# Kernel tuning notes

Hardware: AMD Instinct MI355X
Metric: run time of the kernel (lower is better)

## Reference

```python
import jax, jax.numpy as jnp
import numpy as np

N_QUBITS = 14
N_LAYERS = 6
BATCH = 512
DIM = 2 ** N_QUBITS

# Z expectation sign table: qubit 0 is the most-significant bit of the state index
_idx = np.arange(DIM)
_bits = np.stack([(_idx >> (N_QUBITS - 1 - q)) & 1 for q in range(N_QUBITS)])  # [n, DIM]
SIGNS = jnp.asarray(1.0 - 2.0 * _bits, dtype=jnp.float32)  # +1 for bit 0, -1 for bit 1


def _rx(theta):
    # 2x2 RX(theta) = [[cos(t/2), -i sin(t/2)], [-i sin(t/2), cos(t/2)]]
    c = jnp.cos(theta / 2).astype(jnp.complex64)
    s = ((-1j) * jnp.sin(theta / 2)).astype(jnp.complex64)
    return jnp.stack([jnp.stack([c, s]), jnp.stack([s, c])])


def _apply_1q(state, mat, q):
    # state: [B, 2^n] complex; apply 2x2 mat on qubit q
    left = 2 ** q
    right = 2 ** (N_QUBITS - 1 - q)
    s = state.reshape(-1, left, 2, right)
    s = jnp.einsum('ij,bljr->blir', mat, s)
    return s.reshape(-1, DIM)


def _apply_cnot(state, c, t):
    # CNOT(control=c, target=t): flip target bit where control bit is 1
    hi, lo = (c, t) if c < t else (t, c)
    A = 2 ** hi
    M = 2 ** (lo - hi - 1)
    R = 2 ** (N_QUBITS - 1 - lo)
    s = state.reshape(-1, A, 2, M, 2, R)
    if c < t:
        flipped = jnp.flip(s[:, :, 1:2, :, :, :], axis=4)
        s = jnp.concatenate([s[:, :, 0:1, :, :, :], flipped], axis=2)
    else:
        flipped = jnp.flip(s[:, :, :, :, 1:2, :], axis=2)
        s = jnp.concatenate([s[:, :, :, :, 0:1, :], flipped], axis=4)
    return s.reshape(-1, DIM)


def _forward(x, params):
    B = x.shape[0]
    # angle embedding in X basis: product state of RX(x_q)|0> per qubit
    half = 0.5 * x
    amps = jnp.stack([jnp.cos(half).astype(jnp.complex64),
                      ((-1j) * jnp.sin(half)).astype(jnp.complex64)], axis=-1)  # [B, n, 2]
    state = amps[:, 0]
    for q in range(1, N_QUBITS):
        state = (state[:, :, None] * amps[:, q][:, None, :]).reshape(B, -1)
    # basic_entangling ansatz: per-qubit RX then ring of CNOTs, per layer
    for layer in range(N_LAYERS):
        w = params[layer, 0]  # [n_qubits]
        for q in range(N_QUBITS):
            state = _apply_1q(state, _rx(w[q]), q)
        for q in range(N_QUBITS):
            state = _apply_cnot(state, q, (q + 1) % N_QUBITS)
    # <Z_q> expectation per qubit
    probs = state.real ** 2 + state.imag ** 2  # [B, DIM]
    return probs @ SIGNS.T  # [B, n_qubits]


def setup_inputs():
    key = jax.random.key(0)
    k1, k2 = jax.random.split(key)
    x = jax.random.normal(k1, (BATCH, N_QUBITS), dtype=jnp.float32)
    params = 2.0 * jnp.pi * jax.random.uniform(k2, (N_LAYERS, 1, N_QUBITS), dtype=jnp.float32)
    return {"x": x, "params": params}


def reference(x, params):
    return _forward(x, params)
```

## Files before the change

### kernel.cpp

```cpp
#include <hip/hip_runtime.h>
#include <math.h>


#define NQ 14
#define DIM 16384
#define NLAYERS 6
#define NGATES (NLAYERS * NQ)
#define BATCH 512
#define TB 1024
#define NREP 16
#define NSLICE 16
#define SLICE_B (BATCH / NSLICE)
#define B_PER_WAVE (SLICE_B * 64 / TB)

constexpr int cpopc(unsigned v) { int c = 0; while (v) { c += (int)(v & 1u); v >>= 1; } return c; }

constexpr unsigned cpext(unsigned v, unsigned m) {
    unsigned r = 0; int b = 0;
    for (int pos = 0; pos < 16; ++pos)
        if ((m >> pos) & 1u) { r |= ((v >> pos) & 1u) << b; ++b; }
    return r;
}

struct Tabs {
    unsigned short m[NGATES];
    unsigned short r[NQ];
    int p[NQ];
    int off[NQ + 1];
    unsigned char qb[NQ][NQ];
    int ng[NQ];
    unsigned short gmask[NQ][NGATES];
    unsigned char  gidx[NQ][NGATES];
};

constexpr Tabs gen_tabs() {
    Tabs T{};
    unsigned short C[NQ] = {}, R[NQ] = {};
    for (int q = 0; q < NQ; ++q) { C[q] = (unsigned short)(1u << (NQ - 1 - q)); R[q] = C[q]; }
    for (int l = 0; l < NLAYERS; ++l) {
        for (int q = 0; q < NQ; ++q) T.m[l * NQ + q] = C[q];
        for (int g = 0; g < NQ; ++g) {
            int t = (g + 1) % NQ;
            C[g] ^= C[t];
            R[t] ^= R[g];
        }
    }
    for (int q = 0; q < NQ; ++q) T.r[q] = R[q];
    for (int q = 0; q < NQ; ++q) {
        int cnt = 0;
        for (int pos = 0; pos < NQ; ++pos)
            if ((R[q] >> pos) & 1u) { T.qb[q][cnt] = (unsigned char)(NQ - 1 - pos); ++cnt; }
        T.p[q] = cnt;
    }
    T.off[0] = 0;
    for (int q = 0; q < NQ; ++q) T.off[q + 1] = T.off[q] + (1 << T.p[q]);
    for (int q = 0; q < NQ; ++q) {
        int n = 0;
        for (int g = 0; g < NGATES; ++g) {
            if (cpopc((unsigned)(T.m[g] & R[q])) & 1) {
                T.gmask[q][n] = T.m[g];
                T.gidx[q][n]  = (unsigned char)g;
                ++n;
            }
        }
        T.ng[q] = n;
    }
    return T;
}
constexpr Tabs TAB = gen_tabs();

constexpr int calc_maxp() { int m = 0; for (int q = 0; q < NQ; ++q) if (TAB.p[q] > m) m = TAB.p[q]; return m; }
constexpr int calc_minp() { int m = 99; for (int q = 0; q < NQ; ++q) if (TAB.p[q] < m) m = TAB.p[q]; return m; }
constexpr int MAXP  = calc_maxp();
constexpr int MINP  = calc_minp();
constexpr int TOTAL = TAB.off[NQ];
static_assert(MAXP <= 8, "u = t & (2^p-1) needs p <= 10; replicas sized for p <= 8");
static_assert(MINP >= 1, "r mask must be nonzero");

template<int Q, int I>
__device__ __forceinline__ void gates(const float2* __restrict__ w, int t,
                                      float (&Bx)[16], float (&By)[16])
{
    if constexpr (I < TAB.ng[Q]) {
        constexpr unsigned r  = TAB.r[Q];
        constexpr unsigned nr = (~r) & 0x3FFFu;
        constexpr int      p  = TAB.p[Q];
        constexpr unsigned mg = TAB.gmask[Q][I];
        constexpr unsigned Ag = cpext(mg, r);
        constexpr unsigned Bg = cpext(mg, nr);
        constexpr unsigned Mg = Ag | ((Bg & ((1u << (10 - p)) - 1u)) << p);
        constexpr unsigned Hg = (Bg >> (10 - p)) & 15u;
        const float2 wv = w[I];
        const float si = (__popc((unsigned)t & Mg) & 1) ? -wv.y : wv.y;
        const float c  = wv.x;
        const float nx = Bx[Hg] * c - By[Hg] * si;
        const float ny = Bx[Hg] * si + By[Hg] * c;
        Bx[Hg] = nx; By[Hg] = ny;
        gates<Q, I + 1>(w, t, Bx, By);
    }
}

template<int Q>
__device__ __forceinline__ void build_q(const float2* __restrict__ w,
                                        float* __restrict__ binC,
                                        float* __restrict__ binS, int t)
{
    constexpr int      p       = TAB.p[Q];
    constexpr unsigned lowmask = (1u << p) - 1u;

    float Bx[16], By[16];
    #pragma unroll
    for (int h = 0; h < 16; ++h) { Bx[h] = 1.0f; By[h] = 0.0f; }
    gates<Q, 0>(w, t, Bx, By);

    #pragma unroll
    for (int s = 1; s < 4; s <<= 1) {
        #pragma unroll
        for (int h = 0; h < 16; ++h) {
            if (!(h & s)) {
                const int h1 = h | s;
                const float p1 = Bx[h] * Bx[h1], p2 = By[h] * By[h1];
                const float p3 = Bx[h] * By[h1], p4 = By[h] * Bx[h1];
                Bx[h]  = p1 - p2;  By[h]  = p3 + p4;
                Bx[h1] = p1 + p2;  By[h1] = p4 - p3;
            }
        }
    }
    #pragma unroll
    for (int h = 0; h < 4; ++h) {
        const int h1 = h | 4;
        const float p1 = Bx[h] * Bx[h1], p2 = By[h] * By[h1];
        const float p3 = Bx[h] * By[h1], p4 = By[h] * Bx[h1];
        Bx[h]  = p1 - p2;  By[h]  = p3 + p4;
        Bx[h1] = p1 + p2;  By[h1] = p4 - p3;
    }
    #pragma unroll
    for (int h = 8; h < 12; ++h) {
        const int h1 = h | 4;
        const float p1 = Bx[h] * Bx[h1], p2 = By[h] * By[h1];
        Bx[h]  = p1 - p2;
        Bx[h1] = p1 + p2;
    }

    float fx = 0.0f, fy = 0.0f;
    #pragma unroll
    for (int h = 0; h < 8; ++h) {
        fx = fmaf(Bx[h | 8], Bx[h], fx);
        fy = fmaf(Bx[h | 8], By[h], fy);
    }
    fx *= 2.0f; fy *= 2.0f;

    const unsigned u   = (unsigned)t & lowmask;
    const int      rep = t >> 6;
    float* bc = binC + (rep << MAXP);
    float* bs = binS + (rep << MAXP);

    if constexpr (p >= 6) {
        bc[u] = fx;
        bs[u] = fy;
    } else {
        constexpr unsigned dm = 63u & ~lowmask;
        #pragma unroll
        for (int bb = p; bb < 6; ++bb) {
            fx += __shfl_xor(fx, 1 << bb, 64);
            fy += __shfl_xor(fy, 1 << bb, 64);
        }
        if (((unsigned)t & dm) == 0u) {
            bc[u] = fx;
            bs[u] = fy;
        }
    }
}

template<int Q>
__device__ __forceinline__ void run_q(const float2* __restrict__ w,
                                      float* __restrict__ binC,
                                      float* __restrict__ binS,
                                      float2* __restrict__ tab2,
                                      const float* __restrict__ sxAll,
                                      float* __restrict__ out,
                                      int slice, int t)
{
    build_q<Q>(w, binC, binS, t);
    __syncthreads();

    constexpr int p  = TAB.p[Q];
    constexpr int nb = 1 << p;
    for (int i = t; i < nb; i += TB) {
        float sc = 0.0f, ss = 0.0f;
        #pragma unroll
        for (int rp = 0; rp < NREP; ++rp) {
            sc += binC[(rp << MAXP) + i];
            ss += binS[(rp << MAXP) + i];
        }
        tab2[i] = make_float2(sc, ss);
    }
    __syncthreads();

    const int wave = t >> 6;
    const int lane = t & 63;
    #pragma unroll
    for (int bb = 0; bb < B_PER_WAVE; ++bb) {
        const int bl = wave * B_PER_WAVE + bb;
        const float* xr = sxAll + bl * NQ;
        float xv[p];
        #pragma unroll
        for (int i = 0; i < p; ++i) xv[i] = xr[TAB.qb[Q][i]];

        float acc = 0.0f;
        if constexpr (p >= 6) {
            float A_low = 0.0f;
            #pragma unroll
            for (int i = 0; i < 6; ++i) A_low += ((lane >> i) & 1) ? xv[i] : -xv[i];
            constexpr int HI = 1 << (p - 6);
            #pragma unroll
            for (int j = 0; j < HI; ++j) {
                float A = A_low;
                #pragma unroll
                for (int i = 6; i < p; ++i) A += ((j >> (i - 6)) & 1) ? xv[i] : -xv[i];
                const int u = lane + (j << 6);
                float s, c;
                __sincosf(A, &s, &c);
                const float2 tv = tab2[u];
                acc = fmaf(c, tv.x, fmaf(s, tv.y, acc));
            }
        } else {
            if (lane < nb) {
                float A = 0.0f;
                #pragma unroll
                for (int i = 0; i < p; ++i) A += ((lane >> i) & 1) ? xv[i] : -xv[i];
                float s, c;
                __sincosf(A, &s, &c);
                const float2 tv = tab2[lane];
                acc = fmaf(c, tv.x, fmaf(s, tv.y, acc));
            }
        }

        #pragma unroll
        for (int o = 32; o > 0; o >>= 1)
            acc += __shfl_down(acc, o, 64);
        if (lane == 0)
            out[(slice * SLICE_B + bl) * NQ + Q] = acc * (1.0f / (float)DIM);
    }
}

__global__ __launch_bounds__(TB, 4)
void fused_kernel(const float* __restrict__ x, const float* __restrict__ params,
                  float* __restrict__ out)
{
    __shared__ float2 w[NGATES];
    __shared__ float  binC[NREP << MAXP];
    __shared__ float  binS[NREP << MAXP];
    __shared__ float2 tab2[1 << MAXP];
    __shared__ float  sxAll[SLICE_B * NQ];

    const int q     = blockIdx.x % NQ;
    const int slice = blockIdx.x / NQ;
    const int t     = threadIdx.x;
    const int ng    = TAB.ng[q];

    if (t < ng) {
        const float th = params[(int)TAB.gidx[q][t]];
        float s, c; sincosf(th, &s, &c);
        w[t] = make_float2(c, s);
    }
    for (int i = t; i < (NREP << MAXP); i += TB) { binC[i] = 0.0f; binS[i] = 0.0f; }
    for (int i = t; i < SLICE_B * NQ; i += TB)   sxAll[i] = x[slice * (SLICE_B * NQ) + i];
    __syncthreads();

    switch (q) {
        case 0:  run_q<0 >(w, binC, binS, tab2, sxAll, out, slice, t); break;
        case 1:  run_q<1 >(w, binC, binS, tab2, sxAll, out, slice, t); break;
        case 2:  run_q<2 >(w, binC, binS, tab2, sxAll, out, slice, t); break;
        case 3:  run_q<3 >(w, binC, binS, tab2, sxAll, out, slice, t); break;
        case 4:  run_q<4 >(w, binC, binS, tab2, sxAll, out, slice, t); break;
        case 5:  run_q<5 >(w, binC, binS, tab2, sxAll, out, slice, t); break;
        case 6:  run_q<6 >(w, binC, binS, tab2, sxAll, out, slice, t); break;
        case 7:  run_q<7 >(w, binC, binS, tab2, sxAll, out, slice, t); break;
        case 8:  run_q<8 >(w, binC, binS, tab2, sxAll, out, slice, t); break;
        case 9:  run_q<9 >(w, binC, binS, tab2, sxAll, out, slice, t); break;
        case 10: run_q<10>(w, binC, binS, tab2, sxAll, out, slice, t); break;
        case 11: run_q<11>(w, binC, binS, tab2, sxAll, out, slice, t); break;
        case 12: run_q<12>(w, binC, binS, tab2, sxAll, out, slice, t); break;
        case 13: run_q<13>(w, binC, binS, tab2, sxAll, out, slice, t); break;
    }
}

extern "C" void kernel_launch(void* const* d_in, const int* in_sizes, int n_in,
                              void* d_out, int out_size, void* d_ws, size_t ws_size,
                              hipStream_t stream) {
    const float* x      = (const float*)d_in[0];
    const float* params = (const float*)d_in[1];
    float* out          = (float*)d_out;
    (void)d_ws; (void)ws_size;

    fused_kernel<<<NQ * NSLICE, TB, 0, stream>>>(x, params, out);
}
```

Before: 61.57 us.

## Replace complex gate products with angle sums and unroll batch pair in phase B

Each bin's phase factor is now built by summing signed gate angles and combining them with a Walsh-Hadamard butterfly, followed by sin/cos only at the end. This replaces the per-gate complex multiplications and the shared-memory precomputed cos/sin table. The change also drops the bin zero-initialisation and the initial barrier, reduces only the replica slots that were actually written when p>=6, and hand-unrolls the two batches per wave so their sincos work and reductions interleave. The cost is extra transcendental calls per thread and reliance on the final butterfly syncs to order the sxAll writes.

```diff
diff --git a/kernel.cpp b/kernel.cpp
--- a/kernel.cpp
+++ b/kernel.cpp
@@ -12,6 +12,7 @@
 #define NSLICE 16
 #define SLICE_B (BATCH / NSLICE)
 #define B_PER_WAVE (SLICE_B * 64 / TB)
+static_assert(B_PER_WAVE == 2, "phase B hand-unrolled for 2 batches/wave");
 
 constexpr int cpopc(unsigned v) { int c = 0; while (v) { c += (int)(v & 1u); v >>= 1; } return c; }
 
@@ -78,8 +79,8 @@
 static_assert(MINP >= 1, "r mask must be nonzero");
 
 template<int Q, int I>
-__device__ __forceinline__ void gates(const float2* __restrict__ w, int t,
-                                      float (&Bx)[16], float (&By)[16])
+__device__ __forceinline__ void gates(const float* __restrict__ params, int t,
+                                      float (&P)[16])
 {
     if constexpr (I < TAB.ng[Q]) {
         constexpr unsigned r  = TAB.r[Q];
@@ -90,63 +91,46 @@
         constexpr unsigned Bg = cpext(mg, nr);
         constexpr unsigned Mg = Ag | ((Bg & ((1u << (10 - p)) - 1u)) << p);
         constexpr unsigned Hg = (Bg >> (10 - p)) & 15u;
-        const float2 wv = w[I];
-        const float si = (__popc((unsigned)t & Mg) & 1) ? -wv.y : wv.y;
-        const float c  = wv.x;
-        const float nx = Bx[Hg] * c - By[Hg] * si;
-        const float ny = Bx[Hg] * si + By[Hg] * c;
-        Bx[Hg] = nx; By[Hg] = ny;
-        gates<Q, I + 1>(w, t, Bx, By);
+        const float th = params[(int)TAB.gidx[Q][I]];
+        P[Hg] += (__popc((unsigned)t & Mg) & 1) ? -th : th;
+        gates<Q, I + 1>(params, t, P);
     }
 }
 
 template<int Q>
-__device__ __forceinline__ void build_q(const float2* __restrict__ w,
+__device__ __forceinline__ void build_q(const float* __restrict__ params,
                                         float* __restrict__ binC,
                                         float* __restrict__ binS, int t)
 {
     constexpr int      p       = TAB.p[Q];
     constexpr unsigned lowmask = (1u << p) - 1u;
 
-    float Bx[16], By[16];
+    float P[16];
     #pragma unroll
-    for (int h = 0; h < 16; ++h) { Bx[h] = 1.0f; By[h] = 0.0f; }
-    gates<Q, 0>(w, t, Bx, By);
+    for (int h = 0; h < 16; ++h) P[h] = 0.0f;
+    gates<Q, 0>(params, t, P);
 
     #pragma unroll
-    for (int s = 1; s < 4; s <<= 1) {
+    for (int s = 1; s < 8; s <<= 1) {
         #pragma unroll
         for (int h = 0; h < 16; ++h) {
             if (!(h & s)) {
                 const int h1 = h | s;
-                const float p1 = Bx[h] * Bx[h1], p2 = By[h] * By[h1];
-                const float p3 = Bx[h] * By[h1], p4 = By[h] * Bx[h1];
-                Bx[h]  = p1 - p2;  By[h]  = p3 + p4;
-                Bx[h1] = p1 + p2;  By[h1] = p4 - p3;
-            }
-        }
-    }
-    #pragma unroll
-    for (int h = 0; h < 4; ++h) {
-        const int h1 = h | 4;
-        const float p1 = Bx[h] * Bx[h1], p2 = By[h] * By[h1];
-        const float p3 = Bx[h] * By[h1], p4 = By[h] * Bx[h1];
-        Bx[h]  = p1 - p2;  By[h]  = p3 + p4;
-        Bx[h1] = p1 + p2;  By[h1] = p4 - p3;
-    }
-    #pragma unroll
-    for (int h = 8; h < 12; ++h) {
-        const int h1 = h | 4;
-        const float p1 = Bx[h] * Bx[h1], p2 = By[h] * By[h1];
-        Bx[h]  = p1 - p2;
-        Bx[h1] = p1 + p2;
+                const float a = P[h], b = P[h1];
+                P[h]  = a + b;
+                P[h1] = a - b;
+            }
+        }
     }
 
     float fx = 0.0f, fy = 0.0f;
     #pragma unroll
     for (int h = 0; h < 8; ++h) {
-        fx = fmaf(Bx[h | 8], Bx[h], fx);
-        fy = fmaf(Bx[h | 8], By[h], fy);
+        float sa, ca;
+        __sincosf(P[h], &sa, &ca);
+        const float cb = __cosf(P[h | 8]);
+        fx = fmaf(cb, ca, fx);
+        fy = fmaf(cb, sa, fy);
     }
     fx *= 2.0f; fy *= 2.0f;
 
@@ -173,7 +157,7 @@
 }
 
 template<int Q>
-__device__ __forceinline__ void run_q(const float2* __restrict__ w,
+__device__ __forceinline__ void run_q(const float* __restrict__ params,
                                       float* __restrict__ binC,
                                       float* __restrict__ binS,
                                       float2* __restrict__ tab2,
@@ -181,66 +165,104 @@
                                       float* __restrict__ out,
                                       int slice, int t)
 {
-    build_q<Q>(w, binC, binS, t);
+    build_q<Q>(params, binC, binS, t);
     __syncthreads();
 
     constexpr int p  = TAB.p[Q];
     constexpr int nb = 1 << p;
-    for (int i = t; i < nb; i += TB) {
-        float sc = 0.0f, ss = 0.0f;
-        #pragma unroll
-        for (int rp = 0; rp < NREP; ++rp) {
-            sc += binC[(rp << MAXP) + i];
-            ss += binS[(rp << MAXP) + i];
-        }
-        tab2[i] = make_float2(sc, ss);
+    if constexpr (p >= 6) {
+        constexpr int STRIDE = 1 << (p - 6);
+        constexpr int NW     = NREP / STRIDE;
+        for (int i = t; i < nb; i += TB) {
+            const int r0 = i >> 6;
+            float sc = 0.0f, ss = 0.0f;
+            #pragma unroll
+            for (int c = 0; c < NW; ++c) {
+                const int rp = r0 + c * STRIDE;
+                sc += binC[(rp << MAXP) + i];
+                ss += binS[(rp << MAXP) + i];
+            }
+            tab2[i] = make_float2(sc, ss);
+        }
+    } else {
+        for (int i = t; i < nb; i += TB) {
+            float sc = 0.0f, ss = 0.0f;
+            #pragma unroll
+            for (int rp = 0; rp < NREP; ++rp) {
+                sc += binC[(rp << MAXP) + i];
+                ss += binS[(rp << MAXP) + i];
+            }
+            tab2[i] = make_float2(sc, ss);
+        }
     }
     __syncthreads();
 
     const int wave = t >> 6;
     const int lane = t & 63;
+    const int bl0  = wave * B_PER_WAVE;
+    const float* xr0 = sxAll + bl0 * NQ;
+    const float* xr1 = xr0 + NQ;
+
+    float acc0 = 0.0f, acc1 = 0.0f;
+    if constexpr (p >= 6) {
+        float xv0[p], xv1[p];
+        #pragma unroll
+        for (int i = 0; i < p; ++i) {
+            xv0[i] = xr0[TAB.qb[Q][i]];
+            xv1[i] = xr1[TAB.qb[Q][i]];
+        }
+        float A0 = 0.0f, A1 = 0.0f;
+        #pragma unroll
+        for (int i = 0; i < 6; ++i) {
+            const bool bset = (lane >> i) & 1;
+            A0 += bset ? xv0[i] : -xv0[i];
+            A1 += bset ? xv1[i] : -xv1[i];
+        }
+        constexpr int HI = 1 << (p - 6);
+        #pragma unroll
+        for (int j = 0; j < HI; ++j) {
+            float Aj0 = A0, Aj1 = A1;
+            #pragma unroll
+            for (int i = 6; i < p; ++i) {
+                const bool bset = (j >> (i - 6)) & 1;
+                Aj0 += bset ? xv0[i] : -xv0[i];
+                Aj1 += bset ? xv1[i] : -xv1[i];
+            }
+            const float2 tv = tab2[lane + (j << 6)];
+            float s0, c0, s1, c1;
+            __sincosf(Aj0, &s0, &c0);
+            __sincosf(Aj1, &s1, &c1);
+            acc0 = fmaf(c0, tv.x, fmaf(s0, tv.y, acc0));
+            acc1 = fmaf(c1, tv.x, fmaf(s1, tv.y, acc1));
+        }
+    } else {
+        if (lane < nb) {
+            float A0 = 0.0f, A1 = 0.0f;
+            #pragma unroll
+            for (int i = 0; i < p; ++i) {
+                const bool bset = (lane >> i) & 1;
+                const float x0 = xr0[TAB.qb[Q][i]];
+                const float x1 = xr1[TAB.qb[Q][i]];
+                A0 += bset ? x0 : -x0;
+                A1 += bset ? x1 : -x1;
+            }
+            const float2 tv = tab2[lane];
+            float s0, c0, s1, c1;
+            __sincosf(A0, &s0, &c0);
+            __sincosf(A1, &s1, &c1);
+            acc0 = fmaf(c0, tv.x, fmaf(s0, tv.y, acc0));
+            acc1 = fmaf(c1, tv.x, fmaf(s1, tv.y, acc1));
+        }
+    }
+
     #pragma unroll
-    for (int bb = 0; bb < B_PER_WAVE; ++bb) {
-        const int bl = wave * B_PER_WAVE + bb;
-        const float* xr = sxAll + bl * NQ;
-        float xv[p];
-        #pragma unroll
-        for (int i = 0; i < p; ++i) xv[i] = xr[TAB.qb[Q][i]];
-
-        float acc = 0.0f;
-        if constexpr (p >= 6) {
-            float A_low = 0.0f;
-            #pragma unroll
-            for (int i = 0; i < 6; ++i) A_low += ((lane >> i) & 1) ? xv[i] : -xv[i];
-            constexpr int HI = 1 << (p - 6);
-            #pragma unroll
-            for (int j = 0; j < HI; ++j) {
-                float A = A_low;
-                #pragma unroll
-                for (int i = 6; i < p; ++i) A += ((j >> (i - 6)) & 1) ? xv[i] : -xv[i];
-                const int u = lane + (j << 6);
-                float s, c;
-                __sincosf(A, &s, &c);
-                const float2 tv = tab2[u];
-                acc = fmaf(c, tv.x, fmaf(s, tv.y, acc));
-            }
-        } else {
-            if (lane < nb) {
-                float A = 0.0f;
-                #pragma unroll
-                for (int i = 0; i < p; ++i) A += ((lane >> i) & 1) ? xv[i] : -xv[i];
-                float s, c;
-                __sincosf(A, &s, &c);
-                const float2 tv = tab2[lane];
-                acc = fmaf(c, tv.x, fmaf(s, tv.y, acc));
-            }
-        }
-
-        #pragma unroll
-        for (int o = 32; o > 0; o >>= 1)
-            acc += __shfl_down(acc, o, 64);
-        if (lane == 0)
-            out[(slice * SLICE_B + bl) * NQ + Q] = acc * (1.0f / (float)DIM);
+    for (int o = 32; o > 0; o >>= 1) {
+        acc0 += __shfl_down(acc0, o, 64);
+        acc1 += __shfl_down(acc1, o, 64);
+    }
+    if (lane == 0) {
+        out[(slice * SLICE_B + bl0)     * NQ + Q] = acc0 * (1.0f / (float)DIM);
+        out[(slice * SLICE_B + bl0 + 1) * NQ + Q] = acc1 * (1.0f / (float)DIM);
     }
 }
 
@@ -248,7 +270,6 @@
 void fused_kernel(const float* __restrict__ x, const float* __restrict__ params,
                   float* __restrict__ out)
 {
-    __shared__ float2 w[NGATES];
     __shared__ float  binC[NREP << MAXP];
     __shared__ float  binS[NREP << MAXP];
     __shared__ float2 tab2[1 << MAXP];
@@ -257,32 +278,24 @@
     const int q     = blockIdx.x % NQ;
     const int slice = blockIdx.x / NQ;
     const int t     = threadIdx.x;
-    const int ng    = TAB.ng[q];
-
-    if (t < ng) {
-        const float th = params[(int)TAB.gidx[q][t]];
-        float s, c; sincosf(th, &s, &c);
-        w[t] = make_float2(c, s);
-    }
-    for (int i = t; i < (NREP << MAXP); i += TB) { binC[i] = 0.0f; binS[i] = 0.0f; }
-    for (int i = t; i < SLICE_B * NQ; i += TB)   sxAll[i] = x[slice * (SLICE_B * NQ) + i];
-    __syncthreads();
+
+    for (int i = t; i < SLICE_B * NQ; i += TB) sxAll[i] = x[slice * (SLICE_B * NQ) + i];
 
     switch (q) {
-        case 0:  run_q<0 >(w, binC, binS, tab2, sxAll, out, slice, t); break;
-        case 1:  run_q<1 >(w, binC, binS, tab2, sxAll, out, slice, t); break;
-        case 2:  run_q<2 >(w, binC, binS, tab2, sxAll, out, slice, t); break;
-        case 3:  run_q<3 >(w, binC, binS, tab2, sxAll, out, slice, t); break;
-        case 4:  run_q<4 >(w, binC, binS, tab2, sxAll, out, slice, t); break;
-        case 5:  run_q<5 >(w, binC, binS, tab2, sxAll, out, slice, t); break;
-        case 6:  run_q<6 >(w, binC, binS, tab2, sxAll, out, slice, t); break;
-        case 7:  run_q<7 >(w, binC, binS, tab2, sxAll, out, slice, t); break;
-        case 8:  run_q<8 >(w, binC, binS, tab2, sxAll, out, slice, t); break;
-        case 9:  run_q<9 >(w, binC, binS, tab2, sxAll, out, slice, t); break;
-        case 10: run_q<10>(w, binC, binS, tab2, sxAll, out, slice, t); break;
-        case 11: run_q<11>(w, binC, binS, tab2, sxAll, out, slice, t); break;
-        case 12: run_q<12>(w, binC, binS, tab2, sxAll, out, slice, t); break;
-        case 13: run_q<13>(w, binC, binS, tab2, sxAll, out, slice, t); break;
+        case 0:  run_q<0 >(params, binC, binS, tab2, sxAll, out, slice, t); break;
+        case 1:  run_q<1 >(params, binC, binS, tab2, sxAll, out, slice, t); break;
+        case 2:  run_q<2 >(params, binC, binS, tab2, sxAll, out, slice, t); break;
+        case 3:  run_q<3 >(params, binC, binS, tab2, sxAll, out, slice, t); break;
+        case 4:  run_q<4 >(params, binC, binS, tab2, sxAll, out, slice, t); break;
+        case 5:  run_q<5 >(params, binC, binS, tab2, sxAll, out, slice, t); break;
+        case 6:  run_q<6 >(params, binC, binS, tab2, sxAll, out, slice, t); break;
+        case 7:  run_q<7 >(params, binC, binS, tab2, sxAll, out, slice, t); break;
+        case 8:  run_q<8 >(params, binC, binS, tab2, sxAll, out, slice, t); break;
+        case 9:  run_q<9 >(params, binC, binS, tab2, sxAll, out, slice, t); break;
+        case 10: run_q<10>(params, binC, binS, tab2, sxAll, out, slice, t); break;
+        case 11: run_q<11>(params, binC, binS, tab2, sxAll, out, slice, t); break;
+        case 12: run_q<12>(params, binC, binS, tab2, sxAll, out, slice, t); break;
+        case 13: run_q<13>(params, binC, binS, tab2, sxAll, out, slice, t); break;
     }
 }
 
```

Result: faster. 57.29 us (-7.0%).
